# Kernel optimization log

Hardware: AMD Instinct MI355X
Metric: run time of the kernel (lower is better)

Reference implementation:

```python
import jax, jax.numpy as jnp
import numpy as np

B, C, T = 32, 1536, 2048
BN = 128  # bottleneck channels


def setup_inputs() -> dict:
    key = jax.random.key(0)
    k1, k2, k3, k4, k5, k6 = jax.random.split(key, 6)
    x = jax.random.normal(k1, (B, C, T), dtype=jnp.float32)
    padding_mask = jax.random.randint(k2, (B, T), 0, 2) == 1
    W_tdnn = jax.random.normal(k3, (BN, C), dtype=jnp.float32) * (1.0 / np.sqrt(C))
    b_tdnn = jax.random.normal(k4, (BN,), dtype=jnp.float32) * 0.01
    W_attn = jax.random.normal(k5, (C, BN), dtype=jnp.float32) * (1.0 / np.sqrt(BN))
    b_attn = jax.random.normal(k6, (C,), dtype=jnp.float32) * 0.01
    return {"x": x, "padding_mask": padding_mask, "W_tdnn": W_tdnn,
            "b_tdnn": b_tdnn, "W_attn": W_attn, "b_attn": b_attn}


def reference(x, padding_mask, W_tdnn, b_tdnn, W_attn, b_attn):
    # pointwise conv1 (k=1) == channel-wise matmul: (B,C,T) -> (B,BN,T)
    e = jnp.tanh(jnp.einsum('oc,bct->bot', W_tdnn, x) + b_tdnn[None, :, None])
    # pointwise conv2: (B,BN,T) -> (B,C,T)
    a = jnp.einsum('co,bot->bct', W_attn, e) + b_attn[None, :, None]
    a = jnp.where(padding_mask[:, None, :], -1e9, a)
    alpha = jax.nn.softmax(a, axis=2)  # (B,C,T)
    mean = jnp.sum(alpha * x, axis=2)  # (B,C)
    var = jnp.sum(alpha * (x - mean[:, :, None]) ** 2, axis=2)
    std = jnp.sqrt(jnp.clip(var, 1e-9, None))
    return jnp.concatenate([mean, std], axis=1)  # (B,2C)
```

## Files before the change

### kernel.cpp

```cpp
#include <hip/hip_runtime.h>
#include <math.h>

#define Bn  32
#define Cn  1536
#define Tn  2048
#define BNn 128

typedef __attribute__((ext_vector_type(8))) short bf16x8;
typedef __attribute__((ext_vector_type(4))) float fx4;

__device__ __forceinline__ unsigned int f2bf1(float f) {
    unsigned int u = __float_as_uint(f);
    return (u + 0x7fffu + ((u >> 16) & 1u)) >> 16;
}
__device__ __forceinline__ float fast_tanh(float v) {
    return 1.f - 2.f / (__expf(2.f * v) + 1.f);
}

__global__ void k_prep(const float* __restrict__ W1f, const float* __restrict__ Waf,
                       short* __restrict__ W1b, short* __restrict__ Wab) {
    int i = blockIdx.x * 256 + threadIdx.x;
    if (i < BNn * Cn) {
        W1b[i] = (short)f2bf1(W1f[i]);
        Wab[i] = (short)f2bf1(Waf[i]);
    }
}

__global__ __launch_bounds__(256, 2) void k_gemm1(
    const float* __restrict__ x, const short* __restrict__ W1,
    const float* __restrict__ bias, short* __restrict__ e)
{
    __shared__ short sA[128 * 64];

    const int b    = blockIdx.y;
    const int t0   = blockIdx.x * 128;
    const int tid  = threadIdx.x;
    const int lane = tid & 63;
    const int wv   = tid >> 6;
    const int ln   = lane & 15;
    const int g    = lane >> 4;
    const int wt   = (wv & 1) * 64;
    const int wo   = (wv >> 1) * 64;

    const float* xb = x + (size_t)b * Cn * Tn + t0;

    const int t4 = (tid & 31) * 4;
    const int cq = (tid >> 5) * 4;

    fx4 acc[4][4];
    #pragma unroll
    for (int i = 0; i < 4; ++i)
        #pragma unroll
        for (int j = 0; j < 4; ++j) acc[i][j] = (fx4){0.f, 0.f, 0.f, 0.f};

    for (int k0 = 0; k0 < Cn; k0 += 64) {
        bf16x8 bfr[4][2];
        #pragma unroll
        for (int nn = 0; nn < 4; ++nn)
            #pragma unroll
            for (int kt = 0; kt < 2; ++kt)
                bfr[nn][kt] = *(const bf16x8*)(W1 + (size_t)(wo + nn * 16 + ln) * Cn
                                               + k0 + kt * 32 + g * 8);

        float4 xr[2][4];
        #pragma unroll
        for (int p = 0; p < 2; ++p) {
            const int c = cq + p * 32;
            #pragma unroll
            for (int j = 0; j < 4; ++j)
                xr[p][j] = *(const float4*)(xb + (size_t)(k0 + c + j) * Tn + t4);
        }
        __syncthreads();
        #pragma unroll
        for (int p = 0; p < 2; ++p) {
            const int c   = cq + p * 32;
            const int blk = c >> 3;
            const int sub = c & 7;
            #pragma unroll
            for (int i = 0; i < 4; ++i) {
                const int t = t4 + i;
                unsigned int lo = f2bf1(((const float*)&xr[p][0])[i]) |
                                  (f2bf1(((const float*)&xr[p][1])[i]) << 16);
                unsigned int hi = f2bf1(((const float*)&xr[p][2])[i]) |
                                  (f2bf1(((const float*)&xr[p][3])[i]) << 16);
                const int idx = t * 64 + ((blk ^ (t & 7)) << 3) + sub;
                *(uint2*)(sA + idx) = make_uint2(lo, hi);
            }
        }
        __syncthreads();

        #pragma unroll
        for (int kt = 0; kt < 2; ++kt) {
            bf16x8 af[4];
            #pragma unroll
            for (int mm = 0; mm < 4; ++mm) {
                const int t = wt + mm * 16 + ln;
                af[mm] = *(const bf16x8*)(sA + t * 64 + (((kt * 4 + g) ^ (t & 7)) << 3));
            }
            #pragma unroll
            for (int mm = 0; mm < 4; ++mm)
                #pragma unroll
                for (int nn = 0; nn < 4; ++nn)
                    acc[mm][nn] = __builtin_amdgcn_mfma_f32_16x16x32_bf16(
                        af[mm], bfr[nn][kt], acc[mm][nn], 0, 0, 0);
        }
    }

    float bs[4];
    #pragma unroll
    for (int nn = 0; nn < 4; ++nn) bs[nn] = bias[wo + nn * 16 + ln];

    short* eb = e + ((size_t)b * Tn + t0 + wt) * BNn + wo;
    #pragma unroll
    for (int mm = 0; mm < 4; ++mm)
        #pragma unroll
        for (int nn = 0; nn < 4; ++nn) {
            #pragma unroll
            for (int r = 0; r < 4; ++r) {
                const int t = mm * 16 + g * 4 + r;
                const float v = fast_tanh(acc[mm][nn][r] + bs[nn]);
                eb[(size_t)t * BNn + nn * 16 + ln] = (short)f2bf1(v);
            }
        }
}

__global__ __launch_bounds__(128, 2) void k_attn2(
    const float* __restrict__ x, const short* __restrict__ e,
    const short* __restrict__ Wab, const int* __restrict__ mask,
    float* __restrict__ out)
{
    __shared__ short sE[64 * 128];

    const int b    = blockIdx.y;
    const int c0   = blockIdx.x * 64;
    const int tid  = threadIdx.x;
    const int lane = tid & 63;
    const int wv   = tid >> 6;
    const int ln   = lane & 15;
    const int g    = lane >> 4;
    const int cw   = c0 + wv * 32;

    const float* xb    = x + (size_t)b * Cn * Tn;
    const short* ebase = e + (size_t)b * Tn * BNn;
    const int*   mb    = mask + (size_t)b * Tn;

    bf16x8 af[2][4];
    #pragma unroll
    for (int mt = 0; mt < 2; ++mt)
        #pragma unroll
        for (int kt = 0; kt < 4; ++kt)
            af[mt][kt] = *(const bf16x8*)(Wab + (size_t)(cw + mt * 16 + ln) * BNn
                                          + kt * 32 + g * 8);

    float mS[8], S0[8], S1[8], S2[8];
    #pragma unroll
    for (int s = 0; s < 8; ++s) { mS[s] = -1e30f; S0[s] = 0.f; S1[s] = 0.f; S2[s] = 0.f; }

    for (int t0 = 0; t0 < Tn; t0 += 64) {
        float xv[2][4][4];
        #pragma unroll
        for (int mt = 0; mt < 2; ++mt)
            #pragma unroll
            for (int r = 0; r < 4; ++r) {
                const float* xr = xb + (size_t)(cw + mt * 16 + g * 4 + r) * Tn + t0 + ln;
                #pragma unroll
                for (int nt = 0; nt < 4; ++nt) xv[mt][r][nt] = xr[nt * 16];
            }
        int mv4[4];
        #pragma unroll
        for (int nt = 0; nt < 4; ++nt) mv4[nt] = mb[t0 + nt * 16 + ln];

        uint4 ev[8];
        #pragma unroll
        for (int j = 0; j < 8; ++j) {
            const int p   = j * 128 + tid;
            const int t   = p >> 4;
            const int blk = (tid & 15) ^ (t & 15);
            ev[j] = *(const uint4*)(ebase + (size_t)(t0 + t) * BNn + blk * 8);
        }
        __syncthreads();
        #pragma unroll
        for (int j = 0; j < 8; ++j)
            *(uint4*)(sE + (size_t)(j * 128 + tid) * 8) = ev[j];
        __syncthreads();

        fx4 acc[2][4];
        #pragma unroll
        for (int mt = 0; mt < 2; ++mt)
            #pragma unroll
            for (int nt = 0; nt < 4; ++nt) acc[mt][nt] = (fx4){0.f, 0.f, 0.f, 0.f};

        #pragma unroll
        for (int kt = 0; kt < 4; ++kt) {
            bf16x8 bfr[4];
            #pragma unroll
            for (int nt = 0; nt < 4; ++nt) {
                const int t = nt * 16 + ln;
                bfr[nt] = *(const bf16x8*)(sE + t * 128 + (((kt * 4 + g) ^ (t & 15)) << 3));
            }
            #pragma unroll
            for (int mt = 0; mt < 2; ++mt)
                #pragma unroll
                for (int nt = 0; nt < 4; ++nt)
                    acc[mt][nt] = __builtin_amdgcn_mfma_f32_16x16x32_bf16(
                        af[mt][kt], bfr[nt], acc[mt][nt], 0, 0, 0);
        }

        #pragma unroll
        for (int mt = 0; mt < 2; ++mt)
            #pragma unroll
            for (int r = 0; r < 4; ++r) {
                const int s = mt * 4 + r;
                float a0 = mv4[0] ? -1e9f : acc[mt][0][r];
                float a1 = mv4[1] ? -1e9f : acc[mt][1][r];
                float a2 = mv4[2] ? -1e9f : acc[mt][2][r];
                float a3 = mv4[3] ? -1e9f : acc[mt][3][r];
                const float mc = fmaxf(fmaxf(a0, a1), fmaxf(a2, a3));
                const float mn = fmaxf(mS[s], mc);
                const float sc = __expf(mS[s] - mn);
                const float p0 = __expf(a0 - mn), p1 = __expf(a1 - mn);
                const float p2 = __expf(a2 - mn), p3 = __expf(a3 - mn);
                const float x0 = xv[mt][r][0], x1 = xv[mt][r][1];
                const float x2 = xv[mt][r][2], x3 = xv[mt][r][3];
                S0[s] = S0[s] * sc + (p0 + p1 + p2 + p3);
                S1[s] = S1[s] * sc + (p0 * x0 + p1 * x1 + p2 * x2 + p3 * x3);
                S2[s] = S2[s] * sc + (p0 * x0 * x0 + p1 * x1 * x1 + p2 * x2 * x2 + p3 * x3 * x3);
                mS[s] = mn;
            }
    }

    #pragma unroll
    for (int s = 0; s < 8; ++s) {
        float m = mS[s], s0 = S0[s], s1 = S1[s], s2 = S2[s];
        #pragma unroll
        for (int off = 1; off < 16; off <<= 1) {
            const float mo = __shfl_xor(m, off);
            const float q0 = __shfl_xor(s0, off);
            const float q1 = __shfl_xor(s1, off);
            const float q2 = __shfl_xor(s2, off);
            const float mn = fmaxf(m, mo);
            const float ea = __expf(m - mn), eb2 = __expf(mo - mn);
            s0 = s0 * ea + q0 * eb2;
            s1 = s1 * ea + q1 * eb2;
            s2 = s2 * ea + q2 * eb2;
            m = mn;
        }
        if (ln == 0) {
            const int c = cw + (s >> 2) * 16 + g * 4 + (s & 3);
            const float mean = s1 / s0;
            const float var  = fmaxf(s2 / s0 - mean * mean, 1e-9f);
            out[(size_t)b * (2 * Cn) + c]      = mean;
            out[(size_t)b * (2 * Cn) + Cn + c] = sqrtf(var);
        }
    }
}

extern "C" void kernel_launch(void* const* d_in, const int* in_sizes, int n_in,
                              void* d_out, int out_size, void* d_ws, size_t ws_size,
                              hipStream_t stream) {
    const float* x      = (const float*)d_in[0];
    const int*   mask   = (const int*)d_in[1];
    const float* W_tdnn = (const float*)d_in[2];
    const float* b_tdnn = (const float*)d_in[3];
    const float* W_attn = (const float*)d_in[4];
    float* out = (float*)d_out;

    short* e_bf = (short*)d_ws;
    short* W1b  = (short*)((char*)d_ws + (size_t)Bn * Tn * BNn * 2);
    short* Wab  = W1b + (size_t)BNn * Cn;

    k_prep<<<dim3((BNn * Cn + 255) / 256), 256, 0, stream>>>(W_tdnn, W_attn, W1b, Wab);
    k_gemm1<<<dim3(Tn / 128, Bn), 256, 0, stream>>>(x, W1b, b_tdnn, e_bf);
    k_attn2<<<dim3(Cn / 64, Bn), 128, 0, stream>>>(x, e_bf, Wab, mask, out);
}
```

Baseline: 705.7 us.

## Double-buffer GEMM1 with LDS-staged weights and prefetch x tiles in attention

```diff
diff --git a/kernel.cpp b/kernel.cpp
--- a/kernel.cpp
+++ b/kernel.cpp
@@ -5,6 +5,8 @@
 #define Cn  1536
 #define Tn  2048
 #define BNn 128
+#define KC  64
+#define NCH (Cn / KC)
 
 typedef __attribute__((ext_vector_type(8))) short bf16x8;
 typedef __attribute__((ext_vector_type(4))) float fx4;
@@ -26,11 +28,11 @@
     }
 }
 
-__global__ __launch_bounds__(256, 2) void k_gemm1(
+__global__ __launch_bounds__(256) void k_gemm1(
     const float* __restrict__ x, const short* __restrict__ W1,
     const float* __restrict__ bias, short* __restrict__ e)
 {
-    __shared__ short sA[128 * 64];
+    __shared__ short sAll[2][2][128 * 64];
 
     const int b    = blockIdx.y;
     const int t0   = blockIdx.x * 128;
@@ -43,7 +45,6 @@
     const int wo   = (wv >> 1) * 64;
 
     const float* xb = x + (size_t)b * Cn * Tn + t0;
-
     const int t4 = (tid & 31) * 4;
     const int cq = (tid >> 5) * 4;
 
@@ -53,58 +54,71 @@
         #pragma unroll
         for (int j = 0; j < 4; ++j) acc[i][j] = (fx4){0.f, 0.f, 0.f, 0.f};
 
-    for (int k0 = 0; k0 < Cn; k0 += 64) {
-        bf16x8 bfr[4][2];
-        #pragma unroll
-        for (int nn = 0; nn < 4; ++nn)
-            #pragma unroll
-            for (int kt = 0; kt < 2; ++kt)
-                bfr[nn][kt] = *(const bf16x8*)(W1 + (size_t)(wo + nn * 16 + ln) * Cn
-                                               + k0 + kt * 32 + g * 8);
-
-        float4 xr[2][4];
-        #pragma unroll
-        for (int p = 0; p < 2; ++p) {
-            const int c = cq + p * 32;
-            #pragma unroll
-            for (int j = 0; j < 4; ++j)
-                xr[p][j] = *(const float4*)(xb + (size_t)(k0 + c + j) * Tn + t4);
-        }
+    float4 xr[2][4];
+    uint4  wr[4];
+
+#define LOADX(k0) { \
+    _Pragma("unroll") for (int p = 0; p < 2; ++p) { \
+        const int c = cq + p * 32; \
+        _Pragma("unroll") for (int j = 0; j < 4; ++j) \
+            xr[p][j] = *(const float4*)(xb + (size_t)((k0) + c + j) * Tn + t4); } }
+
+#define LOADW(k0) { \
+    _Pragma("unroll") for (int j = 0; j < 4; ++j) { \
+        const int p = j * 256 + tid; const int o = p >> 3; const int kb = p & 7; \
+        wr[j] = *(const uint4*)(W1 + (size_t)o * Cn + (k0) + kb * 8); } }
+
+#define STAGE(buf) { \
+    short* sA = sAll[buf][0]; short* sW = sAll[buf][1]; \
+    _Pragma("unroll") for (int p = 0; p < 2; ++p) { \
+        const int c = cq + p * 32; const int blk = c >> 3; const int sub = c & 7; \
+        _Pragma("unroll") for (int i = 0; i < 4; ++i) { \
+            const int t = t4 + i; \
+            unsigned int lo = f2bf1(((const float*)&xr[p][0])[i]) | \
+                              (f2bf1(((const float*)&xr[p][1])[i]) << 16); \
+            unsigned int hi = f2bf1(((const float*)&xr[p][2])[i]) | \
+                              (f2bf1(((const float*)&xr[p][3])[i]) << 16); \
+            const int idx = t * 64 + ((blk ^ (t & 7)) << 3) + sub; \
+            *(uint2*)(sA + idx) = make_uint2(lo, hi); } } \
+    _Pragma("unroll") for (int j = 0; j < 4; ++j) { \
+        const int p = j * 256 + tid; const int o = p >> 3; const int kb = p & 7; \
+        *(uint4*)(sW + o * 64 + ((kb ^ (o & 7)) << 3)) = wr[j]; } }
+
+    LOADX(0) LOADW(0)
+    STAGE(0)
+    LOADX(KC) LOADW(KC)
+
+    for (int kc = 0; kc < NCH; ++kc) {
         __syncthreads();
-        #pragma unroll
-        for (int p = 0; p < 2; ++p) {
-            const int c   = cq + p * 32;
-            const int blk = c >> 3;
-            const int sub = c & 7;
-            #pragma unroll
-            for (int i = 0; i < 4; ++i) {
-                const int t = t4 + i;
-                unsigned int lo = f2bf1(((const float*)&xr[p][0])[i]) |
-                                  (f2bf1(((const float*)&xr[p][1])[i]) << 16);
-                unsigned int hi = f2bf1(((const float*)&xr[p][2])[i]) |
-                                  (f2bf1(((const float*)&xr[p][3])[i]) << 16);
-                const int idx = t * 64 + ((blk ^ (t & 7)) << 3) + sub;
-                *(uint2*)(sA + idx) = make_uint2(lo, hi);
-            }
-        }
-        __syncthreads();
-
+        if (kc + 1 < NCH) STAGE((kc + 1) & 1)
+        if (kc + 2 < NCH) { LOADX((kc + 2) * KC) LOADW((kc + 2) * KC) }
+
+        const short* sA = sAll[kc & 1][0];
+        const short* sW = sAll[kc & 1][1];
         #pragma unroll
         for (int kt = 0; kt < 2; ++kt) {
-            bf16x8 af[4];
+            bf16x8 af[4], bf[4];
             #pragma unroll
             for (int mm = 0; mm < 4; ++mm) {
                 const int t = wt + mm * 16 + ln;
                 af[mm] = *(const bf16x8*)(sA + t * 64 + (((kt * 4 + g) ^ (t & 7)) << 3));
+            }
+            #pragma unroll
+            for (int nn = 0; nn < 4; ++nn) {
+                const int o = wo + nn * 16 + ln;
+                bf[nn] = *(const bf16x8*)(sW + o * 64 + (((kt * 4 + g) ^ (o & 7)) << 3));
             }
             #pragma unroll
             for (int mm = 0; mm < 4; ++mm)
                 #pragma unroll
                 for (int nn = 0; nn < 4; ++nn)
                     acc[mm][nn] = __builtin_amdgcn_mfma_f32_16x16x32_bf16(
-                        af[mm], bfr[nn][kt], acc[mm][nn], 0, 0, 0);
-        }
-    }
+                        af[mm], bf[nn], acc[mm][nn], 0, 0, 0);
+        }
+    }
+#undef LOADX
+#undef LOADW
+#undef STAGE
 
     float bs[4];
     #pragma unroll
@@ -114,31 +128,31 @@
     #pragma unroll
     for (int mm = 0; mm < 4; ++mm)
         #pragma unroll
-        for (int nn = 0; nn < 4; ++nn) {
+        for (int nn = 0; nn < 4; ++nn)
             #pragma unroll
             for (int r = 0; r < 4; ++r) {
                 const int t = mm * 16 + g * 4 + r;
                 const float v = fast_tanh(acc[mm][nn][r] + bs[nn]);
                 eb[(size_t)t * BNn + nn * 16 + ln] = (short)f2bf1(v);
             }
-        }
-}
-
-__global__ __launch_bounds__(128, 2) void k_attn2(
+}
+
+__global__ __launch_bounds__(256) void k_attn2(
     const float* __restrict__ x, const short* __restrict__ e,
     const short* __restrict__ Wab, const int* __restrict__ mask,
     float* __restrict__ out)
 {
     __shared__ short sE[64 * 128];
+    __shared__ float sX[128 * 68];
 
     const int b    = blockIdx.y;
-    const int c0   = blockIdx.x * 64;
+    const int c0   = blockIdx.x * 128;
     const int tid  = threadIdx.x;
     const int lane = tid & 63;
-    const int wv   = tid >> 6;
+    const int w    = tid >> 6;
     const int ln   = lane & 15;
     const int g    = lane >> 4;
-    const int cw   = c0 + wv * 32;
+    const int cw   = c0 + w * 32;
 
     const float* xb    = x + (size_t)b * Cn * Tn;
     const short* ebase = e + (size_t)b * Tn * BNn;
@@ -156,33 +170,36 @@
     #pragma unroll
     for (int s = 0; s < 8; ++s) { mS[s] = -1e30f; S0[s] = 0.f; S1[s] = 0.f; S2[s] = 0.f; }
 
+    uint4  ev[4];
+    float4 xr4[8];
+
+#define LOADE(tt0) { \
+    _Pragma("unroll") for (int j = 0; j < 4; ++j) { \
+        const int p = j * 256 + tid; const int t = p >> 4; \
+        const int blk = (p & 15) ^ (t & 15); \
+        ev[j] = *(const uint4*)(ebase + (size_t)((tt0) + t) * BNn + blk * 8); } }
+
+#define LOADXC(tt0) { \
+    _Pragma("unroll") for (int j = 0; j < 8; ++j) { \
+        const int row = j * 16 + (tid >> 4); \
+        xr4[j] = *(const float4*)(xb + (size_t)(c0 + row) * Tn + (tt0) + (tid & 15) * 4); } }
+
+    LOADE(0) LOADXC(0)
+
     for (int t0 = 0; t0 < Tn; t0 += 64) {
-        float xv[2][4][4];
-        #pragma unroll
-        for (int mt = 0; mt < 2; ++mt)
-            #pragma unroll
-            for (int r = 0; r < 4; ++r) {
-                const float* xr = xb + (size_t)(cw + mt * 16 + g * 4 + r) * Tn + t0 + ln;
-                #pragma unroll
-                for (int nt = 0; nt < 4; ++nt) xv[mt][r][nt] = xr[nt * 16];
-            }
+        __syncthreads();
+        #pragma unroll
+        for (int j = 0; j < 4; ++j)
+            *(uint4*)(sE + (size_t)(j * 256 + tid) * 8) = ev[j];
+        #pragma unroll
+        for (int j = 0; j < 8; ++j)
+            *(float4*)(sX + (size_t)(j * 16 + (tid >> 4)) * 68 + (tid & 15) * 4) = xr4[j];
+        __syncthreads();
+
+        if (t0 + 64 < Tn) { LOADE(t0 + 64) LOADXC(t0 + 64) }
         int mv4[4];
         #pragma unroll
         for (int nt = 0; nt < 4; ++nt) mv4[nt] = mb[t0 + nt * 16 + ln];
-
-        uint4 ev[8];
-        #pragma unroll
-        for (int j = 0; j < 8; ++j) {
-            const int p   = j * 128 + tid;
-            const int t   = p >> 4;
-            const int blk = (tid & 15) ^ (t & 15);
-            ev[j] = *(const uint4*)(ebase + (size_t)(t0 + t) * BNn + blk * 8);
-        }
-        __syncthreads();
-        #pragma unroll
-        for (int j = 0; j < 8; ++j)
-            *(uint4*)(sE + (size_t)(j * 128 + tid) * 8) = ev[j];
-        __syncthreads();
 
         fx4 acc[2][4];
         #pragma unroll
@@ -211,6 +228,7 @@
             #pragma unroll
             for (int r = 0; r < 4; ++r) {
                 const int s = mt * 4 + r;
+                const float* xrow = sX + (size_t)(w * 32 + mt * 16 + g * 4 + r) * 68 + ln;
                 float a0 = mv4[0] ? -1e9f : acc[mt][0][r];
                 float a1 = mv4[1] ? -1e9f : acc[mt][1][r];
                 float a2 = mv4[2] ? -1e9f : acc[mt][2][r];
@@ -220,14 +238,15 @@
                 const float sc = __expf(mS[s] - mn);
                 const float p0 = __expf(a0 - mn), p1 = __expf(a1 - mn);
                 const float p2 = __expf(a2 - mn), p3 = __expf(a3 - mn);
-                const float x0 = xv[mt][r][0], x1 = xv[mt][r][1];
-                const float x2 = xv[mt][r][2], x3 = xv[mt][r][3];
+                const float x0 = xrow[0], x1 = xrow[16], x2 = xrow[32], x3 = xrow[48];
                 S0[s] = S0[s] * sc + (p0 + p1 + p2 + p3);
                 S1[s] = S1[s] * sc + (p0 * x0 + p1 * x1 + p2 * x2 + p3 * x3);
                 S2[s] = S2[s] * sc + (p0 * x0 * x0 + p1 * x1 * x1 + p2 * x2 * x2 + p3 * x3 * x3);
                 mS[s] = mn;
             }
     }
+#undef LOADE
+#undef LOADXC
 
     #pragma unroll
     for (int s = 0; s < 8; ++s) {
@@ -271,5 +290,5 @@
 
     k_prep<<<dim3((BNn * Cn + 255) / 256), 256, 0, stream>>>(W_tdnn, W_attn, W1b, Wab);
     k_gemm1<<<dim3(Tn / 128, Bn), 256, 0, stream>>>(x, W1b, b_tdnn, e_bf);
-    k_attn2<<<dim3(Cn / 64, Bn), 128, 0, stream>>>(x, e_bf, Wab, mask, out);
-}
+    k_attn2<<<dim3(Cn / 128, Bn), 256, 0, stream>>>(x, e_bf, Wab, mask, out);
+}
```

New measurement: 825.9 us. +17.0%, slower.
